# Kernel optimization log

Measured on AMD Instinct MI355X. Metric: run time of the kernel, lower is better.

Reference implementation:

```python
import jax, jax.numpy as jnp
import numpy as np

TEMP = 0.1
EDGE_THR = 0.25
PATCH = 16
SAMPLE = 100
EPS = 1e-12


def _split_into_patches(feats, P):
    # replicates torch unfold(2).unfold(3).unfold(4).contiguous().view(B,-1,C,P,P,P)
    B, C, D, H, W = feats.shape
    x = feats.reshape(B, C, D // P, P, H // P, P, W // P, P)
    x = x.transpose(0, 1, 2, 4, 6, 3, 5, 7)  # [B,C,Dp,Hp,Wp,P,P,P]
    return x.reshape(B, -1, C, P, P, P)       # C-order reshape == torch .view on contiguous


def _projector(x, w1, b1, w2, b2):
    # torch Linear: y = x @ W.T + b
    h = jax.nn.relu(jnp.matmul(x, w1.T) + b1)
    return jnp.matmul(h, w2.T) + b2


def _normalize(x, axis):
    n = jnp.sqrt(jnp.sum(x * x, axis=axis, keepdims=True))
    return x / jnp.maximum(n, EPS)


def _conv3d(x, w, b, padding):
    y = jax.lax.conv_general_dilated(
        x, w, window_strides=(1, 1, 1), padding=padding,
        dimension_numbers=('NCDHW', 'OIDHW', 'NCDHW'))
    return y + b[None, :, None, None, None]


def setup_inputs() -> dict:
    key = jax.random.key(0)
    ks = jax.random.split(key, 12)
    B, C, D, H, W = 2, 128, 64, 64, 64
    inp = {
        'anchor_feats': jax.random.normal(ks[0], (B, C, D, H, W), dtype=jnp.float32),
        'positive_feats': jax.random.normal(ks[1], (B, C, D, H, W), dtype=jnp.float32),
        'conv1_w': jax.random.normal(ks[2], (32, C, 3, 3, 3), dtype=jnp.float32) * 0.02,
        'conv1_b': jnp.zeros((32,), dtype=jnp.float32),
        'conv2_w': jax.random.normal(ks[3], (1, 32, 1, 1, 1), dtype=jnp.float32) * 0.1,
        'conv2_b': jnp.zeros((1,), dtype=jnp.float32),
        'proj_w1': jax.random.normal(ks[4], (C, C), dtype=jnp.float32) * (1.0 / np.sqrt(C)),
        'proj_b1': jnp.zeros((C,), dtype=jnp.float32),
        'proj_w2': jax.random.normal(ks[5], (64, C), dtype=jnp.float32) * (1.0 / np.sqrt(C)),
        'proj_b2': jnp.zeros((64,), dtype=jnp.float32),
        'loss_weights': jnp.array([1.0, 0.7], dtype=jnp.float32),
        'voxel_idx': jax.random.permutation(ks[6], PATCH ** 3)[:SAMPLE].astype(jnp.int64),
    }
    return inp


def reference(anchor_feats, positive_feats, conv1_w, conv1_b, conv2_w, conv2_b,
              proj_w1, proj_b1, proj_w2, proj_b2, loss_weights, voxel_idx):
    B, C, D, H, W = anchor_feats.shape
    P = PATCH

    # region classifier: Conv3d(C,32,3,p=1) -> ReLU -> Conv3d(32,1,1) -> Sigmoid
    h = jax.nn.relu(_conv3d(anchor_feats, conv1_w, conv1_b, ((1, 1), (1, 1), (1, 1))))
    region_probs = jax.nn.sigmoid(_conv3d(h, conv2_w, conv2_b, ((0, 0), (0, 0), (0, 0))))
    region_mask = (region_probs > EDGE_THR).astype(jnp.float32)  # [B,1,D,H,W]

    anchor_p = _split_into_patches(anchor_feats, P)    # [B,N,C,P,P,P]
    positive_p = _split_into_patches(positive_feats, P)
    region_p = _split_into_patches(region_mask, P)     # [B,N,1,P,P,P]

    edge_ratio = jnp.mean(region_p, axis=(2, 3, 4, 5))  # [B,N]
    mask_vox = (edge_ratio > 0.6).astype(jnp.float32)
    mask_patch = (edge_ratio < 0.4).astype(jnp.float32)

    # ---- patch-level contrast (vectorized over B,N) ----
    a_vec = jnp.mean(anchor_p, axis=(3, 4, 5))    # [B,N,C]
    p_vec = jnp.mean(positive_p, axis=(3, 4, 5))
    a_proj = _normalize(_projector(a_vec, proj_w1, proj_b1, proj_w2, proj_b2), -1)
    p_proj = _normalize(_projector(p_vec, proj_w1, proj_b1, proj_w2, proj_b2), -1)
    patch_losses = -jnp.sum(a_proj * p_proj, axis=-1) / TEMP  # [B,N]

    # ---- voxel-level contrast (vectorized over B,N) ----
    N = anchor_p.shape[1]
    a_vox = anchor_p.reshape(B, N, C, P ** 3).transpose(0, 1, 3, 2)[:, :, voxel_idx, :]  # [B,N,S,C]
    p_vox = positive_p.reshape(B, N, C, P ** 3).transpose(0, 1, 3, 2)[:, :, voxel_idx, :]
    a_vp = _normalize(_projector(a_vox, proj_w1, proj_b1, proj_w2, proj_b2), -1)  # [B,N,S,64]
    p_vp = _normalize(_projector(p_vox, proj_w1, proj_b1, proj_w2, proj_b2), -1)
    sim = jnp.einsum('bnsd,bntd->bnst', a_vp, p_vp) / TEMP  # [B,N,S,S]
    lse = jax.nn.logsumexp(sim, axis=-1)                    # [B,N,S]
    diag = jnp.diagonal(sim, axis1=-2, axis2=-1)            # [B,N,S]
    vox_losses = jnp.mean(lse - diag, axis=-1)              # [B,N]

    patch_sum = jnp.sum(patch_losses * mask_patch)
    vox_sum = jnp.sum(vox_losses * mask_vox)
    valid = jnp.sum(mask_patch) + jnp.sum(mask_vox)

    total = (loss_weights[0] * patch_sum + loss_weights[1] * vox_sum)
    return jnp.where(valid > 0, total / jnp.maximum(valid, 1.0), 0.0)
```

## Files before the change

### kernel.cpp

```cpp
#include <hip/hip_runtime.h>

using short8 = __attribute__((ext_vector_type(8))) short;
using f32x16 = __attribute__((ext_vector_type(16))) float;

#define THR_LOGIT (-1.0986122886681098f)
#define ZPAGE_OFF 156509184

__device__ __forceinline__ unsigned short f2bf(float f) {
  unsigned u = __float_as_uint(f);
  u = (u + 0x7FFFu + ((u >> 16) & 1u)) >> 16;
  return (unsigned short)u;
}

__device__ __forceinline__ void async_copy16(void* lds, const void* g) {
  __builtin_amdgcn_global_load_lds(
      (const __attribute__((address_space(1))) unsigned int*)g,
      (__attribute__((address_space(3))) unsigned int*)lds, 16, 0, 0);
}

__global__ void __launch_bounds__(256) k_prepinv(const float* __restrict__ c1w,
    const float* __restrict__ pw1, const float* __restrict__ pw2,
    short* __restrict__ wt2, float* __restrict__ w1t, float* __restrict__ w2t,
    const int* __restrict__ vidx, int* __restrict__ inv) {
  int bid = blockIdx.x;
  int t = threadIdx.x;
  if (bid == 528) {
    for (int k = t; k < 4096; k += 256) inv[k] = -1;
    __syncthreads();
    if (t < 100) inv[vidx[t]] = t;
    return;
  }
  int i = bid * 256 + t;
  if (i < 110592) {
    int j8 = i & 7, l31v = (i >> 3) & 31, halfv = (i >> 8) & 1;
    int q = i >> 9;
    int dz = q % 3; q /= 3;
    int dx = q % 3; q /= 3;
    int dy = q % 3; int co8 = q / 3;
    int c = co8 * 16 + halfv * 8 + j8;
    int tap = dz * 9 + dy * 3 + dx;
    wt2[i] = (short)f2bf(c1w[l31v * 3456 + c * 27 + tap]);
  } else if (i < 126976) {
    int i2 = i - 110592; int c = i2 >> 7; int j = i2 & 127;
    w1t[i2] = pw1[j * 128 + c];
  } else if (i < 135168) {
    int i3 = i - 126976; int j = i3 >> 6; int d = i3 & 63;
    w2t[i3] = pw2[d * 128 + j];
  }
}

__device__ __forceinline__ void stage_body(float (*tile)[65], int* mcnt_p, int* mx,
    int* mrow, int bi, int t, const float* __restrict__ src, short* __restrict__ in2,
    float* __restrict__ S4, float* __restrict__ Xmat, const int* __restrict__ inv,
    int vox_row_base) {
  int b = bi >> 8, z = (bi >> 2) & 63, yp = bi & 3;
  int zp = z >> 4, pz = z & 15;
  int cc = t & 127, xh = t >> 7;
  float part0 = 0.f, part1 = 0.f;

  for (int y0 = 0; y0 < 16; ++y0) {
    int y = yp * 16 + y0;
    __syncthreads();
    if (t == 0) *mcnt_p = 0;
    {
      int xq = (t & 15) * 4, w = t >> 4;
      const float* sp = src + (long)b * 128 * 262144 + (long)z * 4096 + (long)y * 64 + xq;
      #pragma unroll
      for (int s = 0; s < 8; ++s) {
        int c = s * 16 + w;
        float4 v = *(const float4*)(sp + (long)c * 262144);
        tile[c][xq + 0] = v.x;
        tile[c][xq + 1] = v.y;
        tile[c][xq + 2] = v.z;
        tile[c][xq + 3] = v.w;
      }
    }
    __syncthreads();
    if (in2 != nullptr) {
      long rowbase = ((long)(b * 64 + z) * 64 + y) * 8192;
      int x = t >> 2, q = t & 3;
      int slot = (q & 1) ^ ((x >> 2) & 1);
      #pragma unroll
      for (int i = 0; i < 4; ++i) {
        int co8 = i * 2 + (q >> 1);
        short8 pk;
        #pragma unroll
        for (int j = 0; j < 8; ++j) pk[j] = (short)f2bf(tile[i * 32 + q * 8 + j][x]);
        *(short8*)(in2 + rowbase + co8 * 1024 + x * 16 + slot * 8) = pk;
      }
    }
    {
      float s0 = 0.f, s1 = 0.f;
      #pragma unroll
      for (int px = 0; px < 16; ++px) s0 += tile[cc][(xh * 2) * 16 + px];
      #pragma unroll
      for (int px = 0; px < 16; ++px) s1 += tile[cc][(xh * 2 + 1) * 16 + px];
      part0 += s0; part1 += s1;
    }
    if (t < 64) {
      int s = inv[pz * 256 + y0 * 16 + (t & 15)];
      if (s >= 0) {
        int idx = atomicAdd(mcnt_p, 1);
        mx[idx] = t;
        int n = zp * 16 + yp * 4 + (t >> 4);
        mrow[idx] = vox_row_base + (b * 64 + n) * 100 + s;
      }
    }
    __syncthreads();
    int mc = *mcnt_p;
    for (int i = 0; i < mc; ++i) {
      if (t < 128) Xmat[(long)mrow[i] * 128 + t] = tile[t][mx[i]];
    }
  }
  long sb = ((long)(b * 64 + z) * 4 + yp) * 512;
  S4[sb + cc * 4 + xh * 2 + 0] = part0;
  S4[sb + cc * 4 + xh * 2 + 1] = part1;
}

__global__ void __launch_bounds__(256) k_stage(const float* __restrict__ src,
    short* __restrict__ in2, float* __restrict__ S4, float* __restrict__ Xmat,
    const int* __restrict__ inv, int vox_row_base) {
  __shared__ float tile[128][65];
  __shared__ int mcnt;
  __shared__ int mx[64];
  __shared__ int mrow[64];
  stage_body(tile, &mcnt, mx, mrow, blockIdx.x, threadIdx.x,
             src, in2, S4, Xmat, inv, vox_row_base);
}

__global__ void __launch_bounds__(256, 2) k_fused(const short* __restrict__ in2,
    const short* __restrict__ wt2, const float* __restrict__ c1b,
    const float* __restrict__ c2w, const float* __restrict__ c2b,
    int* __restrict__ counts,
    const float* __restrict__ positive, float* __restrict__ S4p,
    float* __restrict__ Xmat, const int* __restrict__ inv) {
  extern __shared__ char smem[];
  int bid = blockIdx.x;
  int role = bid % 3;
  int tid = threadIdx.x;

  if (role == 2) {
    int* mcnt_p = (int*)(smem + 33280);
    int* mx = (int*)(smem + 33280 + 4);
    int* mrow = (int*)(smem + 33280 + 4 + 256);
    stage_body((float(*)[65])smem, mcnt_p, mx, mrow, bid / 3, tid,
               positive, nullptr, S4p, Xmat, inv, 13056);
    return;
  }

  int bi0 = (bid / 3) * 2 + role;
  int bi = ((bi0 & 7) << 7) | (bi0 >> 3);
  int b = bi >> 9, zb = (bi >> 4) & 31, yg = bi & 15;
  int z0 = zb * 2, y0 = yg * 4;
  int lane = tid & 63;
  int l31 = lane & 31, half = lane >> 5;
  int wave = tid >> 6;
  int xh = wave & 1, yo = wave >> 1;
  const short8 zer = {};

  int gbase[12];
  int gmask[12];
  #pragma unroll
  for (int k = 0; k < 12; ++k) {
    int g = k * 256 + tid;
    int row = g >> 7, pos = g & 127;
    int zz = z0 - 1 + row / 6;
    int yy = y0 - 1 + row % 6;
    bool v = ((unsigned)zz < 64u) && ((unsigned)yy < 64u);
    gbase[k] = v ? (((b * 64 + zz) * 64 + yy) * 16384 + pos * 16)
                 : (ZPAGE_OFF + pos * 16);
    gmask[k] = v ? -1 : 0;
  }
  const char* gsrc = (const char*)in2;

  int xbase = xh * 32 + l31;
  int offA[3];
  bool vA[3];
  #pragma unroll
  for (int d = 0; d < 3; ++d) {
    int xp = xbase + d - 1;
    vA[d] = (unsigned)xp < 64u;
    int xc = min(max(xp, 0), 63);
    offA[d] = xc * 32 + ((half ^ ((xc >> 2) & 1)) << 4);
  }
  int ybase = yo * 4096;
  const short8* pBbase = (const short8*)wt2 + half * 32 + l31;

  f32x16 acc[2][2] = {};

  #pragma unroll
  for (int k = 0; k < 12; ++k)
    async_copy16(smem + (k * 256 + tid) * 16, gsrc + gbase[k]);
  __syncthreads();

  for (int co8 = 0; co8 < 8; ++co8) {
    #pragma unroll
    for (int dx = 0; dx < 3; ++dx) {
      bool v = vA[dx];
      int o = offA[dx] + ybase;
      short8 A[4][4];
      #pragma unroll
      for (int zs = 0; zs < 4; ++zs)
        #pragma unroll
        for (int yr = 0; yr < 4; ++yr) {
          short8 a = *(const short8*)(smem + (zs * 12288 + yr * 2048) + o);
          A[zs][yr] = v ? a : zer;
        }
      __builtin_amdgcn_s_setprio(1);
      #pragma unroll
      for (int dz = 0; dz < 3; ++dz) {
        #pragma unroll
        for (int dy = 0; dy < 3; ++dy) {
          short8 bf = pBbase[((co8 * 9 + dy * 3 + dx) * 3 + dz) * 64];
          acc[0][0] = __builtin_amdgcn_mfma_f32_32x32x16_bf16(A[dz + 0][dy + 0], bf, acc[0][0], 0, 0, 0);
          acc[1][0] = __builtin_amdgcn_mfma_f32_32x32x16_bf16(A[dz + 1][dy + 0], bf, acc[1][0], 0, 0, 0);
          acc[0][1] = __builtin_amdgcn_mfma_f32_32x32x16_bf16(A[dz + 0][dy + 1], bf, acc[0][1], 0, 0, 0);
          acc[1][1] = __builtin_amdgcn_mfma_f32_32x32x16_bf16(A[dz + 1][dy + 1], bf, acc[1][1], 0, 0, 0);
        }
      }
      __builtin_amdgcn_s_setprio(0);
    }
    __syncthreads();
    if (co8 < 7) {
      int cadd = (co8 + 1) * 2048;
      #pragma unroll
      for (int k = 0; k < 12; ++k)
        async_copy16(smem + (k * 256 + tid) * 16,
                     gsrc + gbase[k] + (cadd & gmask[k]));
      __syncthreads();
    }
  }

  int* lcnt = (int*)smem;
  if (tid < 4) lcnt[tid] = 0;
  __syncthreads();

  float b1v = c1b[l31];
  float w2v = c2w[l31];
  float b2v = c2b[0];
  int cnt0 = 0, cnt1 = 0;
  #pragma unroll
  for (int zi = 0; zi < 2; ++zi) {
    #pragma unroll
    for (int yi = 0; yi < 2; ++yi) {
      #pragma unroll
      for (int r = 0; r < 16; ++r) {
        float v = fmaxf(acc[zi][yi][r] + b1v, 0.f) * w2v;
        v += __shfl_xor(v, 1);
        v += __shfl_xor(v, 2);
        v += __shfl_xor(v, 4);
        v += __shfl_xor(v, 8);
        v += __shfl_xor(v, 16);
        int bit = (v + b2v) > THR_LOGIT;
        if (r < 8) cnt0 += bit; else cnt1 += bit;
      }
    }
  }
  if (l31 == 0) {
    atomicAdd(&lcnt[xh * 2 + 0], cnt0);
    atomicAdd(&lcnt[xh * 2 + 1], cnt1);
  }
  __syncthreads();
  if (tid < 4) {
    int n = (zb >> 3) * 16 + (yg >> 2) * 4 + tid;
    atomicAdd(&counts[b * 64 + n], lcnt[tid]);
  }
}

__global__ void __launch_bounds__(256) k_proj(const float* __restrict__ Xmat,
    const float* __restrict__ S4a, const float* __restrict__ S4p,
    const float* __restrict__ w1t, const float* __restrict__ pb1,
    const float* __restrict__ w2t, const float* __restrict__ pb2,
    float* __restrict__ P) {
  __shared__ float xsT[128][20];
  __shared__ float hsT[128][20];
  __shared__ float os[16][68];
  int bi = blockIdx.x;
  long row0 = (long)bi * 16;
  int t = threadIdx.x;
  if (bi < 16) {
    int r = t >> 4, c0 = (t & 15) * 8;
    int row = (int)row0 + r;
    int ten = row >> 7, rem = row & 127, b = rem >> 6, n = rem & 63;
    int zp = n >> 4, yp = (n >> 2) & 3, xp = n & 3;
    const float* S = ten ? S4p : S4a;
    #pragma unroll
    for (int k8 = 0; k8 < 8; ++k8) {
      int c = c0 + k8;
      float s = 0.f;
      #pragma unroll
      for (int k = 0; k < 16; ++k)
        s += S[((long)(b * 64 + zp * 16 + k) * 4 + yp) * 512 + c * 4 + xp];
      xsT[c][r] = s * (1.f / 4096.f);
    }
  } else {
    int r = t >> 4, c0 = (t & 15) * 8;
    const float* xp = Xmat + (row0 + r) * 128 + c0;
    #pragma unroll
    for (int k = 0; k < 8; ++k) xsT[c0 + k][r] = xp[k];
  }
  __syncthreads();
  {
    int j = t & 127, rh = t >> 7;
    float hacc[8];
    float bb = pb1[j];
    #pragma unroll
    for (int r8 = 0; r8 < 8; ++r8) hacc[r8] = bb;
    for (int c = 0; c < 128; ++c) {
      float w = w1t[c * 128 + j];
      float4 xlo = *(const float4*)&xsT[c][rh * 8];
      float4 xhi = *(const float4*)&xsT[c][rh * 8 + 4];
      hacc[0] += xlo.x * w; hacc[1] += xlo.y * w; hacc[2] += xlo.z * w; hacc[3] += xlo.w * w;
      hacc[4] += xhi.x * w; hacc[5] += xhi.y * w; hacc[6] += xhi.z * w; hacc[7] += xhi.w * w;
    }
    #pragma unroll
    for (int r8 = 0; r8 < 8; ++r8) hsT[j][rh * 8 + r8] = fmaxf(hacc[r8], 0.f);
  }
  __syncthreads();
  {
    int d = t & 63, rq = t >> 6;
    float oacc[4];
    float bb = pb2[d];
    #pragma unroll
    for (int r4 = 0; r4 < 4; ++r4) oacc[r4] = bb;
    for (int j = 0; j < 128; ++j) {
      float w = w2t[j * 64 + d];
      float4 hv = *(const float4*)&hsT[j][rq * 4];
      oacc[0] += hv.x * w; oacc[1] += hv.y * w; oacc[2] += hv.z * w; oacc[3] += hv.w * w;
    }
    #pragma unroll
    for (int r4 = 0; r4 < 4; ++r4) os[rq * 4 + r4][d] = oacc[r4];
  }
  __syncthreads();
  {
    int r = t >> 4, dg = t & 15;
    float4 v = *(const float4*)&os[r][dg * 4];
    float ss = v.x * v.x + v.y * v.y + v.z * v.z + v.w * v.w;
    ss += __shfl_xor(ss, 1); ss += __shfl_xor(ss, 2);
    ss += __shfl_xor(ss, 4); ss += __shfl_xor(ss, 8);
    float sc = 1.f / fmaxf(sqrtf(ss), 1e-12f);
    float4 o; o.x = v.x * sc; o.y = v.y * sc; o.z = v.z * sc; o.w = v.w * sc;
    *(float4*)&P[(row0 + r) * 64 + dg * 4] = o;
  }
}

__global__ void __launch_bounds__(128) k_sim(const float* __restrict__ P,
                                             float* __restrict__ vloss) {
  __shared__ float ps[100][68];
  __shared__ float red[128];
  int bn = blockIdx.x;
  int t = threadIdx.x;
  long pbase = (long)(13056 + bn * 100) * 64;
  for (int i = t; i < 1600; i += 128) {
    int r = i >> 4, dg = i & 15;
    *(float4*)&ps[r][dg * 4] = *(const float4*)&P[pbase + r * 64 + dg * 4];
  }
  float4 areg[16];
  long abase = (long)(256 + bn * 100) * 64;
  if (t < 100) {
    #pragma unroll
    for (int j = 0; j < 16; ++j) areg[j] = *(const float4*)&P[abase + (long)t * 64 + j * 4];
  }
  __syncthreads();
  float res = 0.f;
  if (t < 100) {
    float m = -1e30f, sum = 0.f, diag = 0.f;
    for (int t2 = 0; t2 < 100; ++t2) {
      float d = 0.f;
      #pragma unroll
      for (int j = 0; j < 16; ++j) {
        float4 pv = *(const float4*)&ps[t2][j * 4];
        d += areg[j].x * pv.x + areg[j].y * pv.y + areg[j].z * pv.z + areg[j].w * pv.w;
      }
      float sim = d * 10.f;
      if (t2 == t) diag = sim;
      float nm = fmaxf(m, sim);
      sum = sum * __expf(m - nm) + __expf(sim - nm);
      m = nm;
    }
    res = m + logf(sum) - diag;
  }
  red[t] = res;
  __syncthreads();
  if (t == 0) {
    float s = 0.f;
    for (int i = 0; i < 100; ++i) s += red[i];
    vloss[bn] = s * 0.01f;
  }
}

__global__ void __launch_bounds__(128) k_final(const float* __restrict__ P,
    const float* __restrict__ vloss, const int* __restrict__ counts,
    const float* __restrict__ lw, float* __restrict__ out) {
  int t = threadIdx.x;
  int lane = t & 63;
  float pterm = 0.f, vterm = 0.f; int vcnt = 0;
  {
    int c = counts[t];
    bool maskv = c >= 2458;
    bool maskp = c <= 1638;
    float d = 0.f;
    for (int k = 0; k < 64; ++k) d += P[t * 64 + k] * P[(128 + t) * 64 + k];
    if (maskp) { pterm = -d * 10.f; vcnt += 1; }
    if (maskv) { vterm = vloss[t];  vcnt += 1; }
  }
  for (int m = 1; m < 64; m <<= 1) {
    pterm += __shfl_xor(pterm, m);
    vterm += __shfl_xor(vterm, m);
    vcnt  += __shfl_xor(vcnt, m);
  }
  __shared__ float sp[2], sv[2]; __shared__ int sc[2];
  if (lane == 0) { sp[t >> 6] = pterm; sv[t >> 6] = vterm; sc[t >> 6] = vcnt; }
  __syncthreads();
  if (t == 0) {
    float psum = sp[0] + sp[1], vsum = sv[0] + sv[1];
    int vc = sc[0] + sc[1];
    float total = lw[0] * psum + lw[1] * vsum;
    out[0] = (vc > 0) ? total / (float)vc : 0.f;
  }
}

extern "C" void kernel_launch(void* const* d_in, const int* in_sizes, int n_in,
                              void* d_out, int out_size, void* d_ws, size_t ws_size,
                              hipStream_t stream) {
  const float* anchor   = (const float*)d_in[0];
  const float* positive = (const float*)d_in[1];
  const float* c1w = (const float*)d_in[2];
  const float* c1b = (const float*)d_in[3];
  const float* c2w = (const float*)d_in[4];
  const float* c2b = (const float*)d_in[5];
  const float* pw1 = (const float*)d_in[6];
  const float* pb1 = (const float*)d_in[7];
  const float* pw2 = (const float*)d_in[8];
  const float* pb2 = (const float*)d_in[9];
  const float* lw  = (const float*)d_in[10];
  const int*   vidx = (const int*)d_in[11];

  char* ws = (char*)d_ws;
  short* in2   = (short*)(ws + 0);
  float* S4a   = (float*)(ws + 134217728);
  float* S4p   = (float*)(ws + 135266304);
  float* X     = (float*)(ws + 136314880);
  float* P     = (float*)(ws + 149553152);
  short* wt2   = (short*)(ws + 156172288);
  float* w1t   = (float*)(ws + 156393472);
  float* w2t   = (float*)(ws + 156459008);
  int*   inv   = (int*)  (ws + 156491776);
  int*   counts= (int*)  (ws + 156508160);
  float* vloss = (float*)(ws + 156508672);
  short* zpage = (short*)(ws + ZPAGE_OFF);

  hipFuncSetAttribute(reinterpret_cast<const void*>(k_fused),
                      hipFuncAttributeMaxDynamicSharedMemorySize, 49152);

  hipMemsetAsync(counts, 0, 128 * sizeof(int), stream);
  hipMemsetAsync(zpage, 0, 16384, stream);
  k_prepinv<<<529, 256, 0, stream>>>(c1w, pw1, pw2, wt2, w1t, w2t, vidx, inv);
  k_stage<<<512, 256, 0, stream>>>(anchor, in2, S4a, X, inv, 256);
  k_fused<<<1536, 256, 49152, stream>>>(in2, wt2, c1b, c2w, c2b, counts,
                                        positive, S4p, X, inv);
  k_proj<<<1616, 256, 0, stream>>>(X, S4a, S4p, w1t, pb1, w2t, pb2, P);
  k_sim<<<128, 128, 0, stream>>>(P, vloss);
  k_final<<<1, 128, 0, stream>>>(P, vloss, counts, lw, (float*)d_out);
}
```

Baseline: 379.5 us.

## Split positive staging out of conv kernel and use zero-page LDS for padding

Moves the positive-feature staging work out of the fused conv kernel into a combined anchor/positive staging kernel, so the conv kernel runs only conv blocks. Out-of-range x taps now read from a zeroed 1 KB LDS region through masked address arithmetic instead of using a per-load select. This simplifies the conv inner loop and evens out block work. In exchange, staging of the positive features no longer overlaps with conv compute, and the conv kernel uses slightly more LDS.

```diff
diff --git a/kernel.cpp b/kernel.cpp
--- a/kernel.cpp
+++ b/kernel.cpp
@@ -117,46 +117,43 @@
   S4[sb + cc * 4 + xh * 2 + 1] = part1;
 }
 
-__global__ void __launch_bounds__(256) k_stage(const float* __restrict__ src,
-    short* __restrict__ in2, float* __restrict__ S4, float* __restrict__ Xmat,
-    const int* __restrict__ inv, int vox_row_base) {
+__global__ void __launch_bounds__(256) k_stage2(const float* __restrict__ anchor,
+    const float* __restrict__ positive, short* __restrict__ in2,
+    float* __restrict__ S4a, float* __restrict__ S4p, float* __restrict__ Xmat,
+    const int* __restrict__ inv) {
   __shared__ float tile[128][65];
   __shared__ int mcnt;
   __shared__ int mx[64];
   __shared__ int mrow[64];
-  stage_body(tile, &mcnt, mx, mrow, blockIdx.x, threadIdx.x,
-             src, in2, S4, Xmat, inv, vox_row_base);
-}
-
-__global__ void __launch_bounds__(256, 2) k_fused(const short* __restrict__ in2,
+  int bid = blockIdx.x;
+  int role = bid & 1, bi = bid >> 1;
+  if (role == 0)
+    stage_body(tile, &mcnt, mx, mrow, bi, threadIdx.x,
+               anchor, in2, S4a, Xmat, inv, 256);
+  else
+    stage_body(tile, &mcnt, mx, mrow, bi, threadIdx.x,
+               positive, nullptr, S4p, Xmat, inv, 13056);
+}
+
+__global__ void __launch_bounds__(256, 2) k_conv(const short* __restrict__ in2,
     const short* __restrict__ wt2, const float* __restrict__ c1b,
     const float* __restrict__ c2w, const float* __restrict__ c2b,
-    int* __restrict__ counts,
-    const float* __restrict__ positive, float* __restrict__ S4p,
-    float* __restrict__ Xmat, const int* __restrict__ inv) {
+    int* __restrict__ counts) {
   extern __shared__ char smem[];
-  int bid = blockIdx.x;
-  int role = bid % 3;
-  int tid = threadIdx.x;
-
-  if (role == 2) {
-    int* mcnt_p = (int*)(smem + 33280);
-    int* mx = (int*)(smem + 33280 + 4);
-    int* mrow = (int*)(smem + 33280 + 4 + 256);
-    stage_body((float(*)[65])smem, mcnt_p, mx, mrow, bid / 3, tid,
-               positive, nullptr, S4p, Xmat, inv, 13056);
-    return;
-  }
-
-  int bi0 = (bid / 3) * 2 + role;
+  __shared__ int lcnt[4];
+  int bi0 = blockIdx.x;
   int bi = ((bi0 & 7) << 7) | (bi0 >> 3);
   int b = bi >> 9, zb = (bi >> 4) & 31, yg = bi & 15;
   int z0 = zb * 2, y0 = yg * 4;
+  int tid = threadIdx.x;
   int lane = tid & 63;
   int l31 = lane & 31, half = lane >> 5;
   int wave = tid >> 6;
   int xh = wave & 1, yo = wave >> 1;
-  const short8 zer = {};
+
+  if (tid < 4) lcnt[tid] = 0;
+  *(int*)(smem + 49152 + tid * 4) = 0;
+  int zoff = 49152 + lane * 16;
 
   int gbase[12];
   int gmask[12];
@@ -175,13 +172,14 @@
 
   int xbase = xh * 32 + l31;
   int offA[3];
-  bool vA[3];
+  int vmA[3];
   #pragma unroll
   for (int d = 0; d < 3; ++d) {
     int xp = xbase + d - 1;
-    vA[d] = (unsigned)xp < 64u;
+    bool v = (unsigned)xp < 64u;
     int xc = min(max(xp, 0), 63);
-    offA[d] = xc * 32 + ((half ^ ((xc >> 2) & 1)) << 4);
+    offA[d] = v ? (xc * 32 + ((half ^ ((xc >> 2) & 1)) << 4)) : zoff;
+    vmA[d] = v ? -1 : 0;
   }
   int ybase = yo * 4096;
   const short8* pBbase = (const short8*)wt2 + half * 32 + l31;
@@ -196,16 +194,14 @@
   for (int co8 = 0; co8 < 8; ++co8) {
     #pragma unroll
     for (int dx = 0; dx < 3; ++dx) {
-      bool v = vA[dx];
-      int o = offA[dx] + ybase;
+      int m = vmA[dx], o = offA[dx];
       short8 A[4][4];
       #pragma unroll
       for (int zs = 0; zs < 4; ++zs)
         #pragma unroll
-        for (int yr = 0; yr < 4; ++yr) {
-          short8 a = *(const short8*)(smem + (zs * 12288 + yr * 2048) + o);
-          A[zs][yr] = v ? a : zer;
-        }
+        for (int yr = 0; yr < 4; ++yr)
+          A[zs][yr] = *(const short8*)(smem +
+              (((zs * 12288 + yr * 2048) + ybase) & m) + o);
       __builtin_amdgcn_s_setprio(1);
       #pragma unroll
       for (int dz = 0; dz < 3; ++dz) {
@@ -230,10 +226,6 @@
       __syncthreads();
     }
   }
-
-  int* lcnt = (int*)smem;
-  if (tid < 4) lcnt[tid] = 0;
-  __syncthreads();
 
   float b1v = c1b[l31];
   float w2v = c2w[l31];
@@ -450,15 +442,14 @@
   float* vloss = (float*)(ws + 156508672);
   short* zpage = (short*)(ws + ZPAGE_OFF);
 
-  hipFuncSetAttribute(reinterpret_cast<const void*>(k_fused),
-                      hipFuncAttributeMaxDynamicSharedMemorySize, 49152);
+  hipFuncSetAttribute(reinterpret_cast<const void*>(k_conv),
+                      hipFuncAttributeMaxDynamicSharedMemorySize, 50176);
 
   hipMemsetAsync(counts, 0, 128 * sizeof(int), stream);
   hipMemsetAsync(zpage, 0, 16384, stream);
   k_prepinv<<<529, 256, 0, stream>>>(c1w, pw1, pw2, wt2, w1t, w2t, vidx, inv);
-  k_stage<<<512, 256, 0, stream>>>(anchor, in2, S4a, X, inv, 256);
-  k_fused<<<1536, 256, 49152, stream>>>(in2, wt2, c1b, c2w, c2b, counts,
-                                        positive, S4p, X, inv);
+  k_stage2<<<1024, 256, 0, stream>>>(anchor, positive, in2, S4a, S4p, X, inv);
+  k_conv<<<1024, 256, 50176, stream>>>(in2, wt2, c1b, c2w, c2b, counts);
   k_proj<<<1616, 256, 0, stream>>>(X, S4a, S4p, w1t, pb1, w2t, pb2, P);
   k_sim<<<128, 128, 0, stream>>>(P, vloss);
   k_final<<<1, 128, 0, stream>>>(P, vloss, counts, lw, (float*)d_out);
```

Result: slower. 391.2 us (+3.1%).
